# Kernel tuning notes

Hardware: AMD Instinct MI355X
Metric: run time of the kernel (lower is better)

Reference implementation:

```python
import jax, jax.numpy as jnp
import numpy as np

L, N, D, E, KD = 4, 40000, 128, 320000, 16
DECAY, N_ITER, EPS = 0.5, 3, 1e-5


def setup_inputs() -> dict:
    key = jax.random.key(0)
    ks = jax.random.split(key, 16)
    s = 0.05
    return {
        "x": jax.random.normal(ks[0], (L, N, D), jnp.float32),
        "edge_rows": jax.random.randint(ks[1], (E,), 0, N, jnp.int32),
        "edge_cols": jax.random.randint(ks[2], (E,), 0, N, jnp.int32),
        "edge_vals": jax.random.uniform(ks[3], (E,), jnp.float32) * 0.1,
        "sage_W": jax.random.normal(ks[4], (D, D), jnp.float32) * s,
        "sage_b": jnp.zeros((D,), jnp.float32),
        "sage_agg_W": jax.random.normal(ks[5], (D, D), jnp.float32) * s,
        "key_W": jax.random.normal(ks[6], (D, KD), jnp.float32) * s,
        "query_W": jax.random.normal(ks[7], (D, KD), jnp.float32) * s,
        "value_W": jax.random.normal(ks[8], (D, D), jnp.float32) * s,
        "attn_ln_g": jnp.ones((D,), jnp.float32),
        "attn_ln_b": jnp.zeros((D,), jnp.float32),
        "lin_W": jax.random.normal(ks[9], (D, D), jnp.float32) * s,
        "lin_b": jnp.zeros((D,), jnp.float32),
        "ln_g": jnp.ones((D,), jnp.float32),
        "ln_b": jnp.zeros((D,), jnp.float32),
    }


def _layernorm(x, g, b):
    mu = jnp.mean(x, axis=-1, keepdims=True)
    var = jnp.mean((x - mu) ** 2, axis=-1, keepdims=True)
    return (x - mu) * jax.lax.rsqrt(var + EPS) * g + b


def _spmm(rows, cols, vals, x2d):
    # sparse [N,N] @ dense [N,F]: out[r] = sum_e vals[e] * x2d[cols[e]] for rows[e]==r
    return jax.ops.segment_sum(vals[:, None] * x2d[cols], rows, num_segments=N)


def reference(x, edge_rows, edge_cols, edge_vals, sage_W, sage_b, sage_agg_W,
              key_W, query_W, value_W, attn_ln_g, attn_ln_b,
              lin_W, lin_b, ln_g, ln_b):
    # x: [L, N, D]
    x2d = jnp.transpose(x, (1, 0, 2)).reshape(N, L * D)  # [N, L*D]

    # ---- SAGEConv ----
    proj = x @ sage_W + sage_b
    agg = _spmm(edge_rows, edge_cols, edge_vals, x2d)
    agg = jnp.transpose(agg.reshape(N, L, D), (1, 0, 2)) @ sage_agg_W
    sage_out = jax.nn.silu(proj + agg)

    # ---- RetentiveAttention ----
    weights = jnp.mean((x @ key_W) * (x @ query_W), axis=-1, keepdims=True)
    x_acc = x
    cur = x2d
    for _ in range(1, N_ITER):
        cur = _spmm(edge_rows, edge_cols, edge_vals, cur * DECAY)
        xr = jnp.transpose(cur.reshape(N, L, D), (1, 0, 2))  # [L, N, D]
        weights = weights + jnp.mean((xr @ key_W) * (xr @ query_W), axis=-1, keepdims=True)
        x_acc = x_acc + xr
    attn_out = _layernorm((x_acc @ value_W) * weights, attn_ln_g, attn_ln_b)

    # ---- GPSConv fusion ----
    y = jax.nn.silu((sage_out + attn_out) @ lin_W + lin_b)
    return _layernorm(y, ln_g, ln_b)
```

## Files before the change

### kernel.cpp

```cpp
#include <hip/hip_runtime.h>
#include <math.h>

#define LL 4
#define NN 40000
#define DD 128
#define EE 320000
#define ROWS (LL*NN)
#define ND (NN*DD)
#define EPS_LN 1e-5f

typedef __attribute__((ext_vector_type(8))) short bf16x8;
typedef __attribute__((ext_vector_type(4))) short s16x4;
typedef __attribute__((ext_vector_type(4))) float f32x4;

#define OFF_CNT      0
#define OFF_ROWPTR   40000
#define OFF_ROWOFS   80004
#define OFF_CCOLS    120004
#define OFF_CVALS    440004
#define OFF_WBF      760004
#define OFF_A        829636
#define OFF_B        (OFF_A + ROWS*DD/2)
#define OFF_XBF      (OFF_B + ROWS*DD/2)

#define WB_W0  0
#define WB_W1  32768
#define WB_WV  65536
#define WB_WL  98304
#define WB_K   131072
#define WB_Q   135168
#define WB_LO_BIG 16384
#define WB_LO_KQ  2048
#define WB_LOGICAL 69632

__device__ __forceinline__ unsigned fu(float f) { union { float f; unsigned u; } v; v.f = f; return v.u; }
__device__ __forceinline__ float uf(unsigned u) { union { unsigned u; float f; } v; v.u = u; return v.f; }

__device__ __forceinline__ short f2bf(float f) {
    unsigned u = fu(f);
    unsigned r = u + 0x7fffu + ((u >> 16) & 1u);
    return (short)(r >> 16);
}
__device__ __forceinline__ float bf2f(short h) { return uf(((unsigned)(unsigned short)h) << 16); }
__device__ __forceinline__ void splitbf(float v, short& h, short& l) {
    h = f2bf(v);
    l = f2bf(v - bf2f(h));
}

__device__ __forceinline__ unsigned pack_hi(float a, float b) {
    return (fu(a) >> 16) | (fu(b) & 0xffff0000u);
}
__device__ __forceinline__ float resid(float a) {
    return a - uf(fu(a) & 0xffff0000u);
}

union FragU { bf16x8 v; unsigned u[4]; };

__global__ void k_hist(const int* __restrict__ rows, int* __restrict__ cnt) {
    int e = blockIdx.x * 256 + threadIdx.x;
    if (e < EE) atomicAdd(&cnt[rows[e]], 1);
}

__global__ __launch_bounds__(1024) void k_scan1(const int* __restrict__ cnt,
                                                int* __restrict__ row_ptr,
                                                int* __restrict__ bsum) {
    __shared__ int wtot[16];
    int tid = threadIdx.x, lane = tid & 63, wid = tid >> 6;
    int i = blockIdx.x * 1024 + tid;
    int v = (i < NN) ? cnt[i] : 0;
    int incl = v;
    #pragma unroll
    for (int off = 1; off < 64; off <<= 1) {
        int t = __shfl_up(incl, off);
        if (lane >= off) incl += t;
    }
    if (lane == 63) wtot[wid] = incl;
    __syncthreads();
    if (wid == 0) {
        int wv = (lane < 16) ? wtot[lane] : 0;
        #pragma unroll
        for (int off = 1; off < 16; off <<= 1) {
            int t = __shfl_up(wv, off);
            if (lane >= off) wv += t;
        }
        if (lane < 16) wtot[lane] = wv;
    }
    __syncthreads();
    int excl = ((wid > 0) ? wtot[wid - 1] : 0) + incl - v;
    if (i < NN) row_ptr[i] = excl;
    if (tid == 0) bsum[blockIdx.x] = wtot[15];
}

__global__ void k_scan2(const int* __restrict__ bsum, int* __restrict__ bofs) {
    int lane = threadIdx.x;
    int v = (lane < 40) ? bsum[lane] : 0;
    int incl = v;
    #pragma unroll
    for (int off = 1; off < 64; off <<= 1) {
        int t = __shfl_up(incl, off);
        if (lane >= off) incl += t;
    }
    if (lane < 40) bofs[lane] = incl - v;
    if (lane == 39) bofs[40] = incl;
}

__global__ __launch_bounds__(1024) void k_scan3(const int* __restrict__ bofs,
                                                int* __restrict__ row_ptr,
                                                int* __restrict__ row_ofs) {
    int i = blockIdx.x * 1024 + threadIdx.x;
    int add = bofs[blockIdx.x];
    if (i < NN) {
        int v = row_ptr[i] + add;
        row_ptr[i] = v;
        row_ofs[i] = v;
    }
    if (i == NN) row_ptr[NN] = bofs[40];
}

__global__ void k_scatter(const int* __restrict__ rows, const int* __restrict__ cols,
                          const float* __restrict__ vals, int* __restrict__ row_ofs,
                          int* __restrict__ csr_cols, float* __restrict__ csr_vals) {
    int e = blockIdx.x * 256 + threadIdx.x;
    if (e < EE) {
        int r = rows[e];
        int p = atomicAdd(&row_ofs[r], 1);
        csr_cols[p] = cols[e];
        csr_vals[p] = vals[e];
    }
}

__global__ __launch_bounds__(256) void k_xcast(const float* __restrict__ x, short* __restrict__ o) {
    size_t i = ((size_t)blockIdx.x * 256 + threadIdx.x) * 8;
    f32x4 a = *(const f32x4*)(x + i);
    f32x4 b = *(const f32x4*)(x + i + 4);
    bf16x8 r;
    #pragma unroll
    for (int j = 0; j < 4; ++j) { r[j] = f2bf(a[j]); r[j + 4] = f2bf(b[j]); }
    *(bf16x8*)(o + i) = r;
}

__global__ __launch_bounds__(128) void k_spmm(const short* __restrict__ in,
                                              const int* __restrict__ row_ptr,
                                              const int* __restrict__ ccols,
                                              const float* __restrict__ cvals,
                                              short* __restrict__ out) {
    int r = blockIdx.x;
    int tid = threadIdx.x;
    int l = tid >> 5;
    int d4 = (tid & 31) * 4;
    const short* inl = in + (size_t)l * ND + d4;
    f32x4 acc = {0.f, 0.f, 0.f, 0.f};
    int e0 = row_ptr[r], e1 = row_ptr[r + 1];
    int e = e0;
    for (; e + 8 <= e1; e += 8) {
        float v[8]; s16x4 xv[8];
        #pragma unroll
        for (int j = 0; j < 8; ++j) {
            int c = ccols[e + j];
            v[j] = cvals[e + j];
            xv[j] = *(const s16x4*)(inl + (size_t)c * DD);
        }
        #pragma unroll
        for (int j = 0; j < 8; ++j)
            #pragma unroll
            for (int k = 0; k < 4; ++k) acc[k] += v[j] * bf2f(xv[j][k]);
    }
    for (; e + 4 <= e1; e += 4) {
        float v[4]; s16x4 xv[4];
        #pragma unroll
        for (int j = 0; j < 4; ++j) {
            int c = ccols[e + j];
            v[j] = cvals[e + j];
            xv[j] = *(const s16x4*)(inl + (size_t)c * DD);
        }
        #pragma unroll
        for (int j = 0; j < 4; ++j)
            #pragma unroll
            for (int k = 0; k < 4; ++k) acc[k] += v[j] * bf2f(xv[j][k]);
    }
    for (; e + 2 <= e1; e += 2) {
        int c0 = ccols[e], c1 = ccols[e + 1];
        float v0 = cvals[e], v1 = cvals[e + 1];
        s16x4 x0 = *(const s16x4*)(inl + (size_t)c0 * DD);
        s16x4 x1 = *(const s16x4*)(inl + (size_t)c1 * DD);
        #pragma unroll
        for (int k = 0; k < 4; ++k) { acc[k] += v0 * bf2f(x0[k]); acc[k] += v1 * bf2f(x1[k]); }
    }
    if (e < e1) {
        int c = ccols[e];
        float v = cvals[e];
        s16x4 xv = *(const s16x4*)(inl + (size_t)c * DD);
        #pragma unroll
        for (int k = 0; k < 4; ++k) acc[k] += v * bf2f(xv[k]);
    }
    s16x4 o;
    o[0] = f2bf(acc[0]); o[1] = f2bf(acc[1]); o[2] = f2bf(acc[2]); o[3] = f2bf(acc[3]);
    *(s16x4*)(out + (size_t)l * ND + (size_t)r * DD + d4) = o;
}

__global__ void k_prep(const float* __restrict__ W0, const float* __restrict__ W1,
                       const float* __restrict__ Wv, const float* __restrict__ Wl,
                       const float* __restrict__ Kw, const float* __restrict__ Qw,
                       short* __restrict__ o) {
    int t = blockIdx.x * 256 + threadIdx.x;
    if (t >= WB_LOGICAL) return;
    float v;
    int hi_idx, lo_idx;
    if (t < 65536) {
        int m = t >> 14, idx = t & 16383;
        int nn = idx >> 7, kk = idx & 127;
        const float* M = (m == 0) ? W0 : (m == 1) ? W1 : (m == 2) ? Wv : Wl;
        v = M[kk * 128 + nn];
        hi_idx = m * 32768 + idx;
        lo_idx = hi_idx + WB_LO_BIG;
    } else {
        int t2 = t - 65536;
        int sel = t2 >> 11;
        int idx = t2 & 2047;
        int nn = idx >> 7, kk = idx & 127;
        const float* M = sel ? Qw : Kw;
        v = M[kk * 16 + nn];
        hi_idx = WB_K + sel * 4096 + idx;
        lo_idx = hi_idx + WB_LO_KQ;
    }
    short h, l;
    splitbf(v, h, l);
    o[hi_idx] = h;
    o[lo_idx] = l;
}

#define MFMA(a, b, c) __builtin_amdgcn_mfma_f32_16x16x32_bf16(a, b, c, 0, 0, 0)

__global__ __launch_bounds__(256) void k_dense(
    const float* __restrict__ x, const short* __restrict__ A, const short* __restrict__ B,
    const short* __restrict__ wbf,
    const float* __restrict__ sage_b, const float* __restrict__ attn_g,
    const float* __restrict__ attn_b, const float* __restrict__ lin_b,
    const float* __restrict__ ln_g, const float* __restrict__ ln_b,
    float* __restrict__ out)
{
    __shared__ short zs[4][16 * 128];
    const int tid = threadIdx.x;
    const int w = tid >> 6;
    const int lane = tid & 63;
    const int n = lane & 15;
    const int q = lane >> 4;
    const size_t rowA = (size_t)blockIdx.x * 64 + w * 16 + n;
    char* zb = (char*)&zs[0][0] + w * 4096;

    bf16x8 xh[4], ah[4], ch[4];
    f32x4 kx = {0,0,0,0}, qx = {0,0,0,0};
    f32x4 ka = {0,0,0,0}, qa = {0,0,0,0};
    f32x4 kb = {0,0,0,0}, qb = {0,0,0,0};

    {
        const float* xp = x + rowA * 128 + q * 8;
        const short* ap = A + rowA * 128 + q * 8;
        const short* bp = B + rowA * 128 + q * 8;
        const short* Kp = wbf + WB_K + n * 128 + q * 8;
        const short* Qp = wbf + WB_Q + n * 128 + q * 8;
        #pragma unroll
        for (int s = 0; s < 4; ++s) {
            f32x4 x0 = *(const f32x4*)(xp + s * 32);
            f32x4 x1 = *(const f32x4*)(xp + s * 32 + 4);
            bf16x8 av = *(const bf16x8*)(ap + s * 32);
            bf16x8 bv = *(const bf16x8*)(bp + s * 32);

            f32x4 c0, c1;
            #pragma unroll
            for (int j = 0; j < 4; ++j) {
                c0[j] = x0[j] + 0.5f * bf2f(av[j])     + 0.25f * bf2f(bv[j]);
                c1[j] = x1[j] + 0.5f * bf2f(av[j + 4]) + 0.25f * bf2f(bv[j + 4]);
            }

            FragU fxh, fxl, fch;
            #pragma unroll
            for (int i = 0; i < 2; ++i) {
                fxh.u[i]     = pack_hi(x0[2*i], x0[2*i+1]);
                fxh.u[i + 2] = pack_hi(x1[2*i], x1[2*i+1]);
                fxl.u[i]     = pack_hi(resid(x0[2*i]), resid(x0[2*i+1]));
                fxl.u[i + 2] = pack_hi(resid(x1[2*i]), resid(x1[2*i+1]));
                fch.u[i]     = pack_hi(c0[2*i], c0[2*i+1]);
                fch.u[i + 2] = pack_hi(c1[2*i], c1[2*i+1]);
            }
            xh[s] = fxh.v; ah[s] = av; ch[s] = fch.v;

            bf16x8 bkh = *(const bf16x8*)(Kp + s * 32);
            bf16x8 bkl = *(const bf16x8*)(Kp + WB_LO_KQ + s * 32);
            bf16x8 bqh = *(const bf16x8*)(Qp + s * 32);
            bf16x8 bql = *(const bf16x8*)(Qp + WB_LO_KQ + s * 32);
            kx = MFMA(fxh.v, bkh, kx); kx = MFMA(fxl.v, bkh, kx); kx = MFMA(fxh.v, bkl, kx);
            qx = MFMA(fxh.v, bqh, qx); qx = MFMA(fxl.v, bqh, qx); qx = MFMA(fxh.v, bql, qx);
            ka = MFMA(av, bkh, ka); qa = MFMA(av, bqh, qa);
            kb = MFMA(bv, bkh, kb); qb = MFMA(bv, bqh, qb);
        }
    }

    f32x4 wts;
    #pragma unroll
    for (int r = 0; r < 4; ++r) {
        float p = kx[r] * qx[r] + 0.25f * (ka[r] * qa[r]) + 0.0625f * (kb[r] * qb[r]);
        p += __shfl_xor(p, 1);
        p += __shfl_xor(p, 2);
        p += __shfl_xor(p, 4);
        p += __shfl_xor(p, 8);
        wts[r] = p * (1.f / 16.f);
    }

    f32x4 S[8];
    #pragma unroll
    for (int t = 0; t < 8; ++t) {
        float bv = sage_b[t * 16 + n];
        S[t] = (f32x4){bv, bv, bv, bv};
    }
    #pragma unroll
    for (int s = 0; s < 4; ++s) {
        #pragma unroll
        for (int t = 0; t < 8; ++t) {
            bf16x8 w0h = *(const bf16x8*)(wbf + WB_W0 + (t * 16 + n) * 128 + s * 32 + q * 8);
            S[t] = MFMA(xh[s], w0h, S[t]);
            bf16x8 w1h = *(const bf16x8*)(wbf + WB_W1 + (t * 16 + n) * 128 + s * 32 + q * 8);
            S[t] = MFMA(ah[s], w1h, S[t]);
        }
    }
    #pragma unroll
    for (int t = 0; t < 8; ++t)
        #pragma unroll
        for (int r = 0; r < 4; ++r) {
            float v = S[t][r];
            S[t][r] = v / (1.f + __expf(-v));
        }

    f32x4 V[8];
    #pragma unroll
    for (int t = 0; t < 8; ++t) V[t] = (f32x4){0.f, 0.f, 0.f, 0.f};
    #pragma unroll
    for (int s = 0; s < 4; ++s)
        #pragma unroll
        for (int t = 0; t < 8; ++t) {
            bf16x8 wvh = *(const bf16x8*)(wbf + WB_WV + (t * 16 + n) * 128 + s * 32 + q * 8);
            V[t] = MFMA(ch[s], wvh, V[t]);
        }
    f32x4 s1 = {0,0,0,0}, s2 = {0,0,0,0};
    #pragma unroll
    for (int t = 0; t < 8; ++t)
        #pragma unroll
        for (int r = 0; r < 4; ++r) {
            float v = V[t][r] * wts[r];
            V[t][r] = v;
            s1[r] += v; s2[r] += v * v;
        }
    #pragma unroll
    for (int r = 0; r < 4; ++r) {
        float a1 = s1[r], a2 = s2[r];
        a1 += __shfl_xor(a1, 1); a2 += __shfl_xor(a2, 1);
        a1 += __shfl_xor(a1, 2); a2 += __shfl_xor(a2, 2);
        a1 += __shfl_xor(a1, 4); a2 += __shfl_xor(a2, 4);
        a1 += __shfl_xor(a1, 8); a2 += __shfl_xor(a2, 8);
        s1[r] = a1; s2[r] = a2;
    }
    #pragma unroll
    for (int t = 0; t < 8; ++t) {
        float g = attn_g[t * 16 + n];
        float bb = attn_b[t * 16 + n];
        #pragma unroll
        for (int r = 0; r < 4; ++r) {
            float mu = s1[r] * (1.f / 128.f);
            float var = s2[r] * (1.f / 128.f) - mu * mu;
            float rs = rsqrtf(var + EPS_LN);
            float zval = S[t][r] + (V[t][r] - mu) * rs * g + bb;
            int row = q * 4 + r;
            int byte = (row * 256 + (t * 16 + n) * 2) ^ ((row & 7) << 4);
            *(short*)(zb + byte) = f2bf(zval);
        }
    }

    bf16x8 zh[4];
    #pragma unroll
    for (int s = 0; s < 4; ++s) {
        int byte = (n * 256 + s * 64 + q * 16) ^ ((n & 7) << 4);
        zh[s] = *(const bf16x8*)(zb + byte);
    }
    f32x4 F[8];
    #pragma unroll
    for (int t = 0; t < 8; ++t) {
        float bv = lin_b[t * 16 + n];
        F[t] = (f32x4){bv, bv, bv, bv};
    }
    #pragma unroll
    for (int s = 0; s < 4; ++s)
        #pragma unroll
        for (int t = 0; t < 8; ++t) {
            bf16x8 wlh = *(const bf16x8*)(wbf + WB_WL + (t * 16 + n) * 128 + s * 32 + q * 8);
            F[t] = MFMA(zh[s], wlh, F[t]);
        }
    f32x4 t1 = {0,0,0,0}, t2 = {0,0,0,0};
    #pragma unroll
    for (int t = 0; t < 8; ++t)
        #pragma unroll
        for (int r = 0; r < 4; ++r) {
            float v = F[t][r];
            v = v / (1.f + __expf(-v));
            F[t][r] = v;
            t1[r] += v; t2[r] += v * v;
        }
    #pragma unroll
    for (int r = 0; r < 4; ++r) {
        float a1 = t1[r], a2 = t2[r];
        a1 += __shfl_xor(a1, 1); a2 += __shfl_xor(a2, 1);
        a1 += __shfl_xor(a1, 2); a2 += __shfl_xor(a2, 2);
        a1 += __shfl_xor(a1, 4); a2 += __shfl_xor(a2, 4);
        a1 += __shfl_xor(a1, 8); a2 += __shfl_xor(a2, 8);
        t1[r] = a1; t2[r] = a2;
    }
    #pragma unroll
    for (int t = 0; t < 8; ++t) {
        float g = ln_g[t * 16 + n];
        float bb = ln_b[t * 16 + n];
        #pragma unroll
        for (int r = 0; r < 4; ++r) {
            float mu = t1[r] * (1.f / 128.f);
            float var = t2[r] * (1.f / 128.f) - mu * mu;
            float rs = rsqrtf(var + EPS_LN);
            size_t row = (size_t)blockIdx.x * 64 + w * 16 + q * 4 + r;
            out[row * 128 + t * 16 + n] = (F[t][r] - mu) * rs * g + bb;
        }
    }
}

extern "C" void kernel_launch(void* const* d_in, const int* in_sizes, int n_in,
                              void* d_out, int out_size, void* d_ws, size_t ws_size,
                              hipStream_t stream) {
    const float* x       = (const float*)d_in[0];
    const int*   erows   = (const int*)d_in[1];
    const int*   ecols   = (const int*)d_in[2];
    const float* evals   = (const float*)d_in[3];
    const float* sage_W  = (const float*)d_in[4];
    const float* sage_b  = (const float*)d_in[5];
    const float* sage_aW = (const float*)d_in[6];
    const float* key_W   = (const float*)d_in[7];
    const float* query_W = (const float*)d_in[8];
    const float* value_W = (const float*)d_in[9];
    const float* attn_g  = (const float*)d_in[10];
    const float* attn_b  = (const float*)d_in[11];
    const float* lin_W   = (const float*)d_in[12];
    const float* lin_b   = (const float*)d_in[13];
    const float* ln_g    = (const float*)d_in[14];
    const float* ln_b    = (const float*)d_in[15];
    float* out = (float*)d_out;

    int*   wsi = (int*)d_ws;
    float* wsf = (float*)d_ws;
    int*   cnt      = wsi + OFF_CNT;
    int*   row_ptr  = wsi + OFF_ROWPTR;
    int*   row_ofs  = wsi + OFF_ROWOFS;
    int*   csr_cols = wsi + OFF_CCOLS;
    float* csr_vals = wsf + OFF_CVALS;
    short* wbf      = (short*)(wsf + OFF_WBF);
    short* Abf      = (short*)(wsf + OFF_A);
    short* Bbf      = (short*)(wsf + OFF_B);
    short* Xbf      = (short*)(wsf + OFF_XBF);
    int*   bsum     = (int*)(wsf + OFF_A);
    int*   bofs     = bsum + 64;

    hipMemsetAsync(cnt, 0, NN * sizeof(int), stream);
    k_hist<<<(EE + 255) / 256, 256, 0, stream>>>(erows, cnt);
    k_prep<<<(WB_LOGICAL + 255) / 256, 256, 0, stream>>>(sage_W, sage_aW, value_W, lin_W,
                                                         key_W, query_W, wbf);
    k_xcast<<<ROWS * DD / (256 * 8), 256, 0, stream>>>(x, Xbf);
    k_scan1<<<40, 1024, 0, stream>>>(cnt, row_ptr, bsum);
    k_scan2<<<1, 64, 0, stream>>>(bsum, bofs);
    k_scan3<<<40, 1024, 0, stream>>>(bofs, row_ptr, row_ofs);
    k_scatter<<<(EE + 255) / 256, 256, 0, stream>>>(erows, ecols, evals, row_ofs, csr_cols, csr_vals);

    k_spmm<<<NN, 128, 0, stream>>>(Xbf, row_ptr, csr_cols, csr_vals, Abf);
    k_spmm<<<NN, 128, 0, stream>>>(Abf, row_ptr, csr_cols, csr_vals, Bbf);

    k_dense<<<ROWS / 64, 256, 0, stream>>>(x, Abf, Bbf, wbf, sage_b, attn_g, attn_b,
                                           lin_b, ln_g, ln_b, out);
}
```

Before: 565.4 us.

## Widen SpMM gathers to 16B per lane and cut dense-kernel register pressure

The SpMM kernel now uses one 64-lane wave per row, with each lane gathering 8 bf16 values (16 bytes) instead of 4. This halves the thread count and issues wider loads. The dense kernel stops keeping the silu(SAGE) and value accumulators live together: both are spilled to per-wave LDS as bf16 and recombined with the layernorm when the lin-layer fragments are loaded. A launch-bounds occupancy hint is added. This rounds the SAGE output to bf16 one extra time and adds LDS traffic and shuffles.

```diff
diff --git a/kernel.cpp b/kernel.cpp
--- a/kernel.cpp
+++ b/kernel.cpp
@@ -139,63 +139,52 @@
     *(bf16x8*)(o + i) = r;
 }
 
-__global__ __launch_bounds__(128) void k_spmm(const short* __restrict__ in,
-                                              const int* __restrict__ row_ptr,
-                                              const int* __restrict__ ccols,
-                                              const float* __restrict__ cvals,
-                                              short* __restrict__ out) {
+__global__ __launch_bounds__(64) void k_spmm(const short* __restrict__ in,
+                                             const int* __restrict__ row_ptr,
+                                             const int* __restrict__ ccols,
+                                             const float* __restrict__ cvals,
+                                             short* __restrict__ out) {
     int r = blockIdx.x;
-    int tid = threadIdx.x;
-    int l = tid >> 5;
-    int d4 = (tid & 31) * 4;
-    const short* inl = in + (size_t)l * ND + d4;
-    f32x4 acc = {0.f, 0.f, 0.f, 0.f};
+    int lane = threadIdx.x;
+    int l = lane >> 4;
+    int c8 = (lane & 15) * 8;
+    const short* inl = in + (size_t)l * ND + c8;
+    float acc[8] = {0.f, 0.f, 0.f, 0.f, 0.f, 0.f, 0.f, 0.f};
     int e0 = row_ptr[r], e1 = row_ptr[r + 1];
     int e = e0;
     for (; e + 8 <= e1; e += 8) {
-        float v[8]; s16x4 xv[8];
-        #pragma unroll
-        for (int j = 0; j < 8; ++j) {
-            int c = ccols[e + j];
-            v[j] = cvals[e + j];
-            xv[j] = *(const s16x4*)(inl + (size_t)c * DD);
-        }
+        int cc[8]; float vv[8]; bf16x8 xv[8];
+        #pragma unroll
+        for (int j = 0; j < 8; ++j) { cc[j] = ccols[e + j]; vv[j] = cvals[e + j]; }
+        #pragma unroll
+        for (int j = 0; j < 8; ++j) xv[j] = *(const bf16x8*)(inl + (size_t)cc[j] * DD);
         #pragma unroll
         for (int j = 0; j < 8; ++j)
             #pragma unroll
-            for (int k = 0; k < 4; ++k) acc[k] += v[j] * bf2f(xv[j][k]);
+            for (int k = 0; k < 8; ++k) acc[k] += vv[j] * bf2f(xv[j][k]);
     }
     for (; e + 4 <= e1; e += 4) {
-        float v[4]; s16x4 xv[4];
-        #pragma unroll
-        for (int j = 0; j < 4; ++j) {
-            int c = ccols[e + j];
-            v[j] = cvals[e + j];
-            xv[j] = *(const s16x4*)(inl + (size_t)c * DD);
-        }
+        int cc[4]; float vv[4]; bf16x8 xv[4];
+        #pragma unroll
+        for (int j = 0; j < 4; ++j) { cc[j] = ccols[e + j]; vv[j] = cvals[e + j]; }
+        #pragma unroll
+        for (int j = 0; j < 4; ++j) xv[j] = *(const bf16x8*)(inl + (size_t)cc[j] * DD);
         #pragma unroll
         for (int j = 0; j < 4; ++j)
             #pragma unroll
-            for (int k = 0; k < 4; ++k) acc[k] += v[j] * bf2f(xv[j][k]);
-    }
-    for (; e + 2 <= e1; e += 2) {
-        int c0 = ccols[e], c1 = ccols[e + 1];
-        float v0 = cvals[e], v1 = cvals[e + 1];
-        s16x4 x0 = *(const s16x4*)(inl + (size_t)c0 * DD);
-        s16x4 x1 = *(const s16x4*)(inl + (size_t)c1 * DD);
-        #pragma unroll
-        for (int k = 0; k < 4; ++k) { acc[k] += v0 * bf2f(x0[k]); acc[k] += v1 * bf2f(x1[k]); }
-    }
-    if (e < e1) {
+            for (int k = 0; k < 8; ++k) acc[k] += vv[j] * bf2f(xv[j][k]);
+    }
+    for (; e < e1; ++e) {
         int c = ccols[e];
         float v = cvals[e];
-        s16x4 xv = *(const s16x4*)(inl + (size_t)c * DD);
-        #pragma unroll
-        for (int k = 0; k < 4; ++k) acc[k] += v * bf2f(xv[k]);
-    }
-    s16x4 o;
-    o[0] = f2bf(acc[0]); o[1] = f2bf(acc[1]); o[2] = f2bf(acc[2]); o[3] = f2bf(acc[3]);
-    *(s16x4*)(out + (size_t)l * ND + (size_t)r * DD + d4) = o;
+        bf16x8 xv = *(const bf16x8*)(inl + (size_t)c * DD);
+        #pragma unroll
+        for (int k = 0; k < 8; ++k) acc[k] += v * bf2f(xv[k]);
+    }
+    bf16x8 o;
+    #pragma unroll
+    for (int k = 0; k < 8; ++k) o[k] = f2bf(acc[k]);
+    *(bf16x8*)(out + (size_t)l * ND + (size_t)r * DD + c8) = o;
 }
 
 __global__ void k_prep(const float* __restrict__ W0, const float* __restrict__ W1,
@@ -231,7 +220,7 @@
 
 #define MFMA(a, b, c) __builtin_amdgcn_mfma_f32_16x16x32_bf16(a, b, c, 0, 0, 0)
 
-__global__ __launch_bounds__(256) void k_dense(
+__global__ __launch_bounds__(256, 4) void k_dense(
     const float* __restrict__ x, const short* __restrict__ A, const short* __restrict__ B,
     const short* __restrict__ wbf,
     const float* __restrict__ sage_b, const float* __restrict__ attn_g,
@@ -239,14 +228,15 @@
     const float* __restrict__ ln_g, const float* __restrict__ ln_b,
     float* __restrict__ out)
 {
-    __shared__ short zs[4][16 * 128];
+    __shared__ short pv[4][2][2048];
     const int tid = threadIdx.x;
     const int w = tid >> 6;
     const int lane = tid & 63;
     const int n = lane & 15;
     const int q = lane >> 4;
     const size_t rowA = (size_t)blockIdx.x * 64 + w * 16 + n;
-    char* zb = (char*)&zs[0][0] + w * 4096;
+    char* pB = (char*)&pv[w][0][0];
+    char* vB = (char*)&pv[w][1][0];
 
     bf16x8 xh[4], ah[4], ch[4];
     f32x4 kx = {0,0,0,0}, qx = {0,0,0,0};
@@ -307,79 +297,111 @@
         wts[r] = p * (1.f / 16.f);
     }
 
-    f32x4 S[8];
-    #pragma unroll
-    for (int t = 0; t < 8; ++t) {
-        float bv = sage_b[t * 16 + n];
-        S[t] = (f32x4){bv, bv, bv, bv};
-    }
-    #pragma unroll
-    for (int s = 0; s < 4; ++s) {
+    {
+        f32x4 S[8];
         #pragma unroll
         for (int t = 0; t < 8; ++t) {
-            bf16x8 w0h = *(const bf16x8*)(wbf + WB_W0 + (t * 16 + n) * 128 + s * 32 + q * 8);
-            S[t] = MFMA(xh[s], w0h, S[t]);
-            bf16x8 w1h = *(const bf16x8*)(wbf + WB_W1 + (t * 16 + n) * 128 + s * 32 + q * 8);
-            S[t] = MFMA(ah[s], w1h, S[t]);
-        }
-    }
-    #pragma unroll
-    for (int t = 0; t < 8; ++t)
+            float bv = sage_b[t * 16 + n];
+            S[t] = (f32x4){bv, bv, bv, bv};
+        }
+        #pragma unroll
+        for (int s = 0; s < 4; ++s) {
+            #pragma unroll
+            for (int t = 0; t < 8; ++t) {
+                bf16x8 w0h = *(const bf16x8*)(wbf + WB_W0 + (t * 16 + n) * 128 + s * 32 + q * 8);
+                S[t] = MFMA(xh[s], w0h, S[t]);
+                bf16x8 w1h = *(const bf16x8*)(wbf + WB_W1 + (t * 16 + n) * 128 + s * 32 + q * 8);
+                S[t] = MFMA(ah[s], w1h, S[t]);
+            }
+        }
+        #pragma unroll
+        for (int t = 0; t < 8; ++t)
+            #pragma unroll
+            for (int r = 0; r < 4; ++r) {
+                float v = S[t][r];
+                v = v / (1.f + __expf(-v));
+                int row = q * 4 + r;
+                int byte = (row * 256 + (t * 16 + n) * 2) ^ ((row & 7) << 4);
+                *(short*)(pB + byte) = f2bf(v);
+            }
+    }
+
+    float mu_n, rs_n;
+    {
+        f32x4 V[8];
+        #pragma unroll
+        for (int t = 0; t < 8; ++t) V[t] = (f32x4){0.f, 0.f, 0.f, 0.f};
+        #pragma unroll
+        for (int s = 0; s < 4; ++s)
+            #pragma unroll
+            for (int t = 0; t < 8; ++t) {
+                bf16x8 wvh = *(const bf16x8*)(wbf + WB_WV + (t * 16 + n) * 128 + s * 32 + q * 8);
+                V[t] = MFMA(ch[s], wvh, V[t]);
+            }
+        f32x4 s1 = {0,0,0,0}, s2 = {0,0,0,0};
+        #pragma unroll
+        for (int t = 0; t < 8; ++t)
+            #pragma unroll
+            for (int r = 0; r < 4; ++r) {
+                float v = V[t][r] * wts[r];
+                V[t][r] = v;
+                s1[r] += v; s2[r] += v * v;
+            }
         #pragma unroll
         for (int r = 0; r < 4; ++r) {
-            float v = S[t][r];
-            S[t][r] = v / (1.f + __expf(-v));
-        }
-
-    f32x4 V[8];
-    #pragma unroll
-    for (int t = 0; t < 8; ++t) V[t] = (f32x4){0.f, 0.f, 0.f, 0.f};
-    #pragma unroll
-    for (int s = 0; s < 4; ++s)
-        #pragma unroll
-        for (int t = 0; t < 8; ++t) {
-            bf16x8 wvh = *(const bf16x8*)(wbf + WB_WV + (t * 16 + n) * 128 + s * 32 + q * 8);
-            V[t] = MFMA(ch[s], wvh, V[t]);
-        }
-    f32x4 s1 = {0,0,0,0}, s2 = {0,0,0,0};
-    #pragma unroll
-    for (int t = 0; t < 8; ++t)
+            float a1 = s1[r], a2 = s2[r];
+            a1 += __shfl_xor(a1, 1); a2 += __shfl_xor(a2, 1);
+            a1 += __shfl_xor(a1, 2); a2 += __shfl_xor(a2, 2);
+            a1 += __shfl_xor(a1, 4); a2 += __shfl_xor(a2, 4);
+            a1 += __shfl_xor(a1, 8); a2 += __shfl_xor(a2, 8);
+            s1[r] = a1; s2[r] = a2;
+        }
+        float mu4[4], rs4[4];
         #pragma unroll
         for (int r = 0; r < 4; ++r) {
-            float v = V[t][r] * wts[r];
-            V[t][r] = v;
-            s1[r] += v; s2[r] += v * v;
-        }
-    #pragma unroll
-    for (int r = 0; r < 4; ++r) {
-        float a1 = s1[r], a2 = s2[r];
-        a1 += __shfl_xor(a1, 1); a2 += __shfl_xor(a2, 1);
-        a1 += __shfl_xor(a1, 2); a2 += __shfl_xor(a2, 2);
-        a1 += __shfl_xor(a1, 4); a2 += __shfl_xor(a2, 4);
-        a1 += __shfl_xor(a1, 8); a2 += __shfl_xor(a2, 8);
-        s1[r] = a1; s2[r] = a2;
-    }
-    #pragma unroll
-    for (int t = 0; t < 8; ++t) {
-        float g = attn_g[t * 16 + n];
-        float bb = attn_b[t * 16 + n];
-        #pragma unroll
-        for (int r = 0; r < 4; ++r) {
-            float mu = s1[r] * (1.f / 128.f);
-            float var = s2[r] * (1.f / 128.f) - mu * mu;
-            float rs = rsqrtf(var + EPS_LN);
-            float zval = S[t][r] + (V[t][r] - mu) * rs * g + bb;
-            int row = q * 4 + r;
-            int byte = (row * 256 + (t * 16 + n) * 2) ^ ((row & 7) << 4);
-            *(short*)(zb + byte) = f2bf(zval);
-        }
+            mu4[r] = s1[r] * (1.f / 128.f);
+            float var = s2[r] * (1.f / 128.f) - mu4[r] * mu4[r];
+            rs4[r] = rsqrtf(var + EPS_LN);
+        }
+        #pragma unroll
+        for (int t = 0; t < 8; ++t)
+            #pragma unroll
+            for (int r = 0; r < 4; ++r) {
+                int row = q * 4 + r;
+                int byte = (row * 256 + (t * 16 + n) * 2) ^ ((row & 7) << 4);
+                *(short*)(vB + byte) = f2bf(V[t][r]);
+            }
+        int src = (n >> 2) << 4;
+        float mA = __shfl(mu4[0], src), mB_ = __shfl(mu4[1], src);
+        float mC = __shfl(mu4[2], src), mD = __shfl(mu4[3], src);
+        float rA = __shfl(rs4[0], src), rB_ = __shfl(rs4[1], src);
+        float rC = __shfl(rs4[2], src), rD = __shfl(rs4[3], src);
+        float m01 = (n & 1) ? mB_ : mA, m23 = (n & 1) ? mD : mC;
+        float r01 = (n & 1) ? rB_ : rA, r23 = (n & 1) ? rD : rC;
+        mu_n = (n & 2) ? m23 : m01;
+        rs_n = (n & 2) ? r23 : r01;
     }
 
     bf16x8 zh[4];
     #pragma unroll
     for (int s = 0; s < 4; ++s) {
         int byte = (n * 256 + s * 64 + q * 16) ^ ((n & 7) << 4);
-        zh[s] = *(const bf16x8*)(zb + byte);
+        bf16x8 ph = *(const bf16x8*)(pB + byte);
+        bf16x8 vh = *(const bf16x8*)(vB + byte);
+        const float* gp = attn_g + s * 32 + q * 8;
+        const float* bp = attn_b + s * 32 + q * 8;
+        f32x4 g0 = *(const f32x4*)gp, g1 = *(const f32x4*)(gp + 4);
+        f32x4 b0 = *(const f32x4*)bp, b1 = *(const f32x4*)(bp + 4);
+        float z[8];
+        #pragma unroll
+        for (int j = 0; j < 4; ++j) {
+            z[j]     = bf2f(ph[j])     + (bf2f(vh[j])     - mu_n) * rs_n * g0[j] + b0[j];
+            z[j + 4] = bf2f(ph[j + 4]) + (bf2f(vh[j + 4]) - mu_n) * rs_n * g1[j] + b1[j];
+        }
+        FragU f;
+        f.u[0] = pack_hi(z[0], z[1]); f.u[1] = pack_hi(z[2], z[3]);
+        f.u[2] = pack_hi(z[4], z[5]); f.u[3] = pack_hi(z[6], z[7]);
+        zh[s] = f.v;
     }
     f32x4 F[8];
     #pragma unroll
@@ -473,8 +495,8 @@
     k_scan3<<<40, 1024, 0, stream>>>(bofs, row_ptr, row_ofs);
     k_scatter<<<(EE + 255) / 256, 256, 0, stream>>>(erows, ecols, evals, row_ofs, csr_cols, csr_vals);
 
-    k_spmm<<<NN, 128, 0, stream>>>(Xbf, row_ptr, csr_cols, csr_vals, Abf);
-    k_spmm<<<NN, 128, 0, stream>>>(Abf, row_ptr, csr_cols, csr_vals, Bbf);
+    k_spmm<<<NN, 64, 0, stream>>>(Xbf, row_ptr, csr_cols, csr_vals, Abf);
+    k_spmm<<<NN, 64, 0, stream>>>(Abf, row_ptr, csr_cols, csr_vals, Bbf);
 
     k_dense<<<ROWS / 64, 256, 0, stream>>>(x, Abf, Bbf, wbf, sage_b, attn_g, attn_b,
                                            lin_b, ln_g, ln_b, out);
```

Result: slower. 597.8 us (+5.7%).
